# Performance work log

Hardware: AMD Instinct MI355X
Metric: run time of the kernel (lower is better)

Reference implementation:

```python
import jax, jax.numpy as jnp
import numpy as np

HEADS = 20  # SDXL-style: hidden_size 1280 / head_dim 64
IP_SCALE = 1.0


def setup_inputs() -> dict:
    key = jax.random.key(0)
    ks = jax.random.split(key, 12)
    B, Sq, T, C, D, NIP = 4, 4096, 77, 1280, 2048, 16
    s = lambda fan: 1.0 / np.sqrt(fan)
    # post-softmax multiplicative mask: col 0 (sot token) forced to 1, rest a binary spatial mask
    spat = (jax.random.uniform(ks[0], (1, Sq, 1)) < 0.5).astype(jnp.float32)
    attention_mask = jnp.concatenate([jnp.ones((1, Sq, 1)), jnp.tile(spat, (1, 1, T - 1))], axis=-1)
    return {
        "hidden_states": jax.random.normal(ks[1], (B, Sq, C), jnp.float32),
        "encoder_hidden_states": jax.random.normal(ks[2], (B, T, D), jnp.float32),
        "ip_hidden_states": jax.random.normal(ks[3], (B, NIP, D), jnp.float32),
        "attention_mask": attention_mask,
        "Wq": jax.random.normal(ks[4], (C, C), jnp.float32) * s(C),
        "Wk": jax.random.normal(ks[5], (D, C), jnp.float32) * s(D),
        "Wv": jax.random.normal(ks[6], (D, C), jnp.float32) * s(D),
        "Wo": jax.random.normal(ks[7], (C, C), jnp.float32) * s(C),
        "bo": jnp.zeros((C,), jnp.float32),
        "Wk_ip": jax.random.normal(ks[8], (D, C), jnp.float32) * s(D),
        "Wv_ip": jax.random.normal(ks[9], (D, C), jnp.float32) * s(D),
    }


def reference(hidden_states, encoder_hidden_states, ip_hidden_states, attention_mask,
              Wq, Wk, Wv, Wo, bo, Wk_ip, Wv_ip):
    B, Sq, C = hidden_states.shape
    H = HEADS
    d = C // H
    scale = d ** -0.5
    # projections (torch Linear with weights stored [in, out])
    q = (hidden_states @ Wq).reshape(B, Sq, H, d)
    k = (encoder_hidden_states @ Wk).reshape(B, -1, H, d)
    v = (encoder_hidden_states @ Wv).reshape(B, -1, H, d)
    # explicit QK^T softmax, then POST-softmax multiplicative mask (as in get_attention_scores + mask multiply)
    scores = jnp.einsum('bqhd,bkhd->bhqk', q, k) * scale
    probs = jax.nn.softmax(scores, axis=-1)
    probs = probs * attention_mask[:, None, :, :]  # [1,1,Sq,T] broadcast over batch*heads
    out = jnp.einsum('bhqk,bkhd->bqhd', probs, v).reshape(B, Sq, C)
    out = out @ Wo + bo  # to_out[0]; to_out[1] is dropout (identity at eval)
    # IP-adapter stream (single stream, no spatial ip mask): standard SDPA against ip tokens
    k_ip = (ip_hidden_states @ Wk_ip).reshape(B, -1, H, d)
    v_ip = (ip_hidden_states @ Wv_ip).reshape(B, -1, H, d)
    s_ip = jnp.einsum('bqhd,bkhd->bhqk', q, k_ip) * scale
    p_ip = jax.nn.softmax(s_ip, axis=-1)
    ip_out = jnp.einsum('bhqk,bkhd->bqhd', p_ip, v_ip).reshape(B, Sq, C)
    return out + IP_SCALE * ip_out
```

## Files before the change

kernel.cpp:

```cpp
#include <hip/hip_runtime.h>

typedef __attribute__((ext_vector_type(4))) float f32x4;
typedef __attribute__((ext_vector_type(8))) short s16x8;
typedef __attribute__((ext_vector_type(8))) __bf16 bf16x8;
typedef unsigned short u16;

__device__ __forceinline__ u16 f2b(float f) {
  union { float f; unsigned u; } x; x.f = f;
  unsigned r = x.u + 0x7fffu + ((x.u >> 16) & 1u);
  return (u16)(r >> 16);
}
__device__ __forceinline__ float b2f(u16 u) {
  union { unsigned u; float f; } x; x.u = ((unsigned)u) << 16;
  return x.f;
}
__device__ __forceinline__ void gld16(const void* g, void* l) {
  __builtin_amdgcn_global_load_lds(
      (const __attribute__((address_space(1))) unsigned int*)g,
      (__attribute__((address_space(3))) unsigned int*)l, 16, 0, 0);
}
__device__ __forceinline__ f32x4 mfma_bf16(s16x8 a, s16x8 b, f32x4 c) {
  return __builtin_amdgcn_mfma_f32_16x16x32_bf16(
      __builtin_bit_cast(bf16x8, a), __builtin_bit_cast(bf16x8, b), c, 0, 0, 0);
}

#define BAR() asm volatile("s_barrier" ::: "memory")

__global__ void k_convert_all(const float* __restrict__ hs, const float* __restrict__ ehs,
                              const float* __restrict__ iph,
                              u16* __restrict__ hsb, u16* __restrict__ ehsb,
                              u16* __restrict__ ipb) {
  const int n1 = 16384 * 1280 / 4, n2 = 308 * 2048 / 4, n3 = 64 * 2048 / 4;
  int i = blockIdx.x * blockDim.x + threadIdx.x;
  const float* src; u16* dst; int j = i;
  if (i < n1) { src = hs; dst = hsb; }
  else if (i < n1 + n2) { src = ehs; dst = ehsb; j = i - n1; }
  else if (i < n1 + n2 + n3) { src = iph; dst = ipb; j = i - n1 - n2; }
  else return;
  float4 v = ((const float4*)src)[j];
  ushort4 o;
  o.x = f2b(v.x); o.y = f2b(v.y); o.z = f2b(v.z); o.w = f2b(v.w);
  ((ushort4*)dst)[j] = o;
}

__global__ void k_transpose_all(const float* Wk, const float* Wv, const float* Wkip,
                                const float* Wvip, const float* Wq, const float* Wo,
                                u16* TK, u16* TV, u16* TKip, u16* TVip,
                                u16* TQ, u16* TO) {
  const int z = blockIdx.z;
  const float* W = (z == 0) ? Wk : (z == 1) ? Wv : (z == 2) ? Wkip
                  : (z == 3) ? Wvip : (z == 4) ? Wq : Wo;
  u16* T = (z == 0) ? TK : (z == 1) ? TV : (z == 2) ? TKip
          : (z == 3) ? TVip : (z == 4) ? TQ : TO;
  const int K = (z < 4) ? 2048 : 1280;
  const int N = 1280;
  __shared__ float tile[32][33];
  int n0 = blockIdx.x * 32, k0 = blockIdx.y * 32;
  if (k0 >= K) return;
  int tx = threadIdx.x & 31, ty = threadIdx.x >> 5;
#pragma unroll
  for (int i = 0; i < 32; i += 8)
    tile[ty + i][tx] = W[(size_t)(k0 + ty + i) * N + n0 + tx];
  __syncthreads();
#pragma unroll
  for (int i = 0; i < 32; i += 8)
    T[(size_t)(n0 + ty + i) * K + k0 + tx] = f2b(tile[tx][ty + i]);
}

__device__ __forceinline__ void gemm_core0(
    const u16* __restrict__ A, const u16* __restrict__ BT,
    int M, int N, int K, u16* __restrict__ outb, int m0, int n0) {
  const int tid = threadIdx.x;
  const int l = tid & 63;
  const int w = tid >> 6;
  const int wr = w >> 1, wc = w & 1;
  __shared__ u16 As[5][4096];
  __shared__ u16 Bs[5][4096];
  f32x4 acc[4][4] = {};

  const int o0 = tid * 16;
  const int o1 = o0 + 4096;
  const int ra0 = o0 >> 6, ca0 = (o0 & 63) >> 1;
  const int ra1 = o1 >> 6, ca1 = (o1 & 63) >> 1;
  int ga0 = m0 + ra0; if (ga0 >= M) ga0 = M - 1;
  int ga1 = m0 + ra1; if (ga1 >= M) ga1 = M - 1;
  const u16* Ar0 = A + (size_t)ga0 * K + ca0;
  const u16* Ar1 = A + (size_t)ga1 * K + ca1;
  const u16* Br0 = BT + (size_t)(n0 + ra0) * K + ca0;
  const u16* Br1 = BT + (size_t)(n0 + ra1) * K + ca1;

  const int KT = K >> 5;
#define SSTAGE(s, kt)                                 \
  {                                                   \
    const int k0_ = (kt) << 5;                        \
    gld16(Ar0 + k0_, &As[s][o0 >> 1]);                \
    gld16(Ar1 + k0_, &As[s][o1 >> 1]);                \
    gld16(Br0 + k0_, &Bs[s][o0 >> 1]);                \
    gld16(Br1 + k0_, &Bs[s][o1 >> 1]);                \
  }
  SSTAGE(0, 0);
  SSTAGE(1, 1);
  SSTAGE(2, 2);
  SSTAGE(3, 3);
  asm volatile("s_waitcnt vmcnt(12)" ::: "memory");
  BAR();

  int slot = 0, s4 = 4;
  for (int j = 0; j < KT; ++j) {
    if (j + 4 < KT) SSTAGE(s4, j + 4);
    s16x8 af[4], bfr[4];
#pragma unroll
    for (int mi = 0; mi < 4; ++mi)
      af[mi] = *(const s16x8*)&As[slot][(wr * 64 + mi * 16 + (l & 15)) * 32 + (l >> 4) * 8];
#pragma unroll
    for (int ni = 0; ni < 4; ++ni)
      bfr[ni] = *(const s16x8*)&Bs[slot][(wc * 64 + ni * 16 + (l & 15)) * 32 + (l >> 4) * 8];
#pragma unroll
    for (int mi = 0; mi < 4; ++mi)
#pragma unroll
      for (int ni = 0; ni < 4; ++ni)
        acc[mi][ni] = mfma_bf16(af[mi], bfr[ni], acc[mi][ni]);
    const int rem = KT - 2 - j;
    if (rem >= 3)      asm volatile("s_waitcnt vmcnt(12)" ::: "memory");
    else if (rem == 2) asm volatile("s_waitcnt vmcnt(8)" ::: "memory");
    else if (rem == 1) asm volatile("s_waitcnt vmcnt(4)" ::: "memory");
    else               asm volatile("s_waitcnt vmcnt(0)" ::: "memory");
    BAR();
    ++slot; if (slot >= 5) slot = 0;
    ++s4; if (s4 >= 5) s4 = 0;
  }

#pragma unroll
  for (int mi = 0; mi < 4; ++mi) {
    const int mbase = m0 + wr * 64 + mi * 16 + (l >> 4) * 4;
#pragma unroll
    for (int ni = 0; ni < 4; ++ni) {
      const int ncol = n0 + wc * 64 + ni * 16 + (l & 15);
#pragma unroll
      for (int r = 0; r < 4; ++r) {
        int m = mbase + r;
        if (m < M) outb[(size_t)m * N + ncol] = f2b(acc[mi][ni][r]);
      }
    }
  }
#undef SSTAGE
}

__global__ __launch_bounds__(256) void k_gemm_small4(
    const u16* __restrict__ ehsb, const u16* __restrict__ ipb,
    const u16* __restrict__ WkT, const u16* __restrict__ WvT,
    const u16* __restrict__ WkipT, const u16* __restrict__ WvipT,
    u16* kbuf, u16* vbuf, u16* kipb, u16* vipb) {
  const int z = blockIdx.z;
  const int M = (z < 2) ? 308 : 64;
  const int m0 = blockIdx.y * 128;
  if (m0 >= M) return;
  const u16* A = (z < 2) ? ehsb : ipb;
  const u16* BT = (z == 0) ? WkT : (z == 1) ? WvT : (z == 2) ? WkipT : WvipT;
  u16* out = (z == 0) ? kbuf : (z == 1) ? vbuf : (z == 2) ? kipb : vipb;
  gemm_core0(A, BT, M, 1280, 2048, out, m0, blockIdx.x * 128);
}

__global__ void k_vtrans(const u16* __restrict__ vbuf, const u16* __restrict__ vipb,
                         u16* __restrict__ vt, u16* __restrict__ vipt) {
  const int b = blockIdx.x, h = blockIdx.y, z = blockIdx.z;
  const int tid = threadIdx.x;
  __shared__ u16 tile[80][72];
  if (z == 0) {
    for (int s = tid; s < 80 * 8; s += 256) {
      int t = s >> 3, c = s & 7;
      int4 v = {0, 0, 0, 0};
      if (t < 77) v = *(const int4*)(vbuf + (size_t)(b * 77 + t) * 1280 + h * 64 + c * 8);
      *(int4*)&tile[t][c * 8] = v;
    }
    __syncthreads();
    for (int s = tid; s < 64 * 12; s += 256) {
      int d = s / 12, tc = s % 12;
      s16x8 v;
#pragma unroll
      for (int j = 0; j < 8; ++j) {
        int t = tc * 8 + j;
        v[j] = (t < 80) ? (short)tile[t][d] : (short)0;
      }
      *(s16x8*)(vt + ((size_t)(h * 64 + d) * 4 + b) * 96 + tc * 8) = v;
    }
  } else {
    for (int s = tid; s < 16 * 8; s += 256) {
      int t = s >> 3, c = s & 7;
      *(int4*)&tile[t][c * 8] =
          *(const int4*)(vipb + (size_t)(b * 16 + t) * 1280 + h * 64 + c * 8);
    }
    __syncthreads();
    for (int s = tid; s < 64 * 2; s += 256) {
      int d = s >> 1, tc = s & 1;
      s16x8 v;
#pragma unroll
      for (int j = 0; j < 8; ++j) v[j] = (short)tile[tc * 8 + j][d];
      *(s16x8*)(vipt + ((size_t)(h * 64 + d) * 4 + b) * 16 + tc * 8) = v;
    }
  }
}

template <int EPI>
__global__ __launch_bounds__(512, 1) void k_gemm256(
    const u16* __restrict__ A, const u16* __restrict__ BT,
    int N, int K, float alpha,
    u16* __restrict__ outb, float* __restrict__ outf,
    const float* __restrict__ bias, const u16* __restrict__ ipadd,
    int nbx) {
  __shared__ u16 lds[73728];
  const int tid = threadIdx.x, l = tid & 63, w = tid >> 6;
  const int lr = l & 15, lg = l >> 4;
  const int wr = w >> 2, wc = w & 3;
  const bool wlo = (w < 4);

  const int nwg = gridDim.x;
  const int q = nwg >> 3, r = nwg & 7;
  const int xcd = blockIdx.x & 7, lid = blockIdx.x >> 3;
  const int wg = (xcd < r) ? (xcd * (q + 1) + lid)
                           : (r * (q + 1) + (xcd - r) * q + lid);
  const int bm0 = (wg / nbx) * 256, bn0 = (wg % nbx) * 320;

  const int srow = tid >> 2;
  const int sslot = ((tid & 3) ^ ((srow >> 1) & 3)) * 8;
  const size_t aO0 = (size_t)(bm0 + srow) * K + sslot;
  const size_t aO1 = aO0 + (size_t)128 * K;
  const size_t bO0 = (size_t)(bn0 + srow) * K + sslot;
  const size_t bO1 = bO0 + (size_t)128 * K;
  const size_t bO2 = bO0 + (size_t)256 * K;
  const int d0 = tid * 8, d1 = (tid + 512) * 8, d2 = (tid + 1024) * 8;

  const int KT = K >> 5;
  f32x4 acc[8][5] = {};
  s16x8 bfv[5], afv[4];

  const int xsw = (lg ^ ((lr >> 1) & 3)) * 8;
  const int aRow = (wr * 128 + lr) * 32 + xsw;
  const int bRow = 32768 + (wc * 80 + lr) * 32 + xsw;

#define STAGE_A(slot, kt)                                              \
  {                                                                    \
    const int base_ = (slot) * 8192;                                   \
    const size_t go_ = (size_t)(kt) * 32;                              \
    gld16(A + aO0 + go_, &lds[base_ + d0]);                            \
    gld16(A + aO1 + go_, &lds[base_ + d1]);                            \
  }
#define STAGE_B(slot, kt)                                              \
  {                                                                    \
    const int base_ = 32768 + (slot) * 10240;                          \
    const size_t go_ = (size_t)(kt) * 32;                              \
    gld16(BT + bO0 + go_, &lds[base_ + d0]);                           \
    gld16(BT + bO1 + go_, &lds[base_ + d1]);                           \
    if (wlo) gld16(BT + bO2 + go_, &lds[base_ + d2]);                  \
  }
#define WAIT_DEEP()                                                    \
  {                                                                    \
    if (wlo) asm volatile("s_waitcnt vmcnt(10)" ::: "memory");         \
    else     asm volatile("s_waitcnt vmcnt(8)" ::: "memory");          \
  }
#define WAIT_MID()                                                     \
  {                                                                    \
    if (wlo) asm volatile("s_waitcnt vmcnt(5)" ::: "memory");          \
    else     asm volatile("s_waitcnt vmcnt(4)" ::: "memory");          \
  }
#define WAITVM0() asm volatile("s_waitcnt vmcnt(0)" ::: "memory")

  STAGE_A(0, 0); STAGE_B(0, 0);
  STAGE_A(1, 1); STAGE_B(1, 1);
  STAGE_A(2, 2); STAGE_B(2, 2);
  WAIT_DEEP();
  BAR();

  for (int j = 0; j < KT; ++j) {
    const int slot = j & 3;
    const int ab = slot * 8192;
    const int bb = slot * 10240;
    const bool pf = (j + 3 < KT);
    const int s3 = (j + 3) & 3;
#pragma unroll
    for (int ni = 0; ni < 5; ++ni)
      bfv[ni] = *(const s16x8*)&lds[bb + bRow + ni * 512];
#pragma unroll
    for (int mi = 0; mi < 4; ++mi)
      afv[mi] = *(const s16x8*)&lds[ab + aRow + mi * 512];
    if (pf) STAGE_A(s3, j + 3);
    __builtin_amdgcn_s_setprio(1);
#pragma unroll
    for (int mi = 0; mi < 4; ++mi)
#pragma unroll
      for (int ni = 0; ni < 5; ++ni)
        acc[mi][ni] = mfma_bf16(afv[mi], bfv[ni], acc[mi][ni]);
    __builtin_amdgcn_s_setprio(0);
#pragma unroll
    for (int mi = 0; mi < 4; ++mi)
      afv[mi] = *(const s16x8*)&lds[ab + aRow + (mi + 4) * 512];
    if (pf) STAGE_B(s3, j + 3);
    __builtin_amdgcn_s_setprio(1);
#pragma unroll
    for (int mi = 0; mi < 4; ++mi)
#pragma unroll
      for (int ni = 0; ni < 5; ++ni)
        acc[mi + 4][ni] = mfma_bf16(afv[mi], bfv[ni], acc[mi + 4][ni]);
    __builtin_amdgcn_s_setprio(0);
    if (pf) { WAIT_DEEP(); }
    else if (j == KT - 3) { WAIT_MID(); }
    else { WAITVM0(); }
    BAR();
  }

  WAITVM0();
  __syncthreads();

  if constexpr (EPI == 0) {
#pragma unroll
    for (int half = 0; half < 2; ++half) {
      if (half) __syncthreads();
      if (wr == half) {
#pragma unroll
        for (int mi = 0; mi < 8; ++mi) {
          const int row = mi * 16 + lg * 4;
#pragma unroll
          for (int ni = 0; ni < 5; ++ni) {
            const int col = wc * 80 + ni * 16 + lr;
#pragma unroll
            for (int rr = 0; rr < 4; ++rr)
              lds[(row + rr) * 320 + col] = f2b(acc[mi][ni][rr] * alpha);
          }
        }
      }
      __syncthreads();
      const int rbase = tid >> 3;
      const int cseg = tid & 7;
#pragma unroll
      for (int rr2 = 0; rr2 < 2; ++rr2)
#pragma unroll
        for (int jj = 0; jj < 5; ++jj) {
          const int row = rr2 * 64 + rbase;
          const int ch = cseg + jj * 8;
          *(int4*)(outb + (size_t)(bm0 + half * 128 + row) * N + bn0 + ch * 8) =
              *(const int4*)&lds[row * 320 + ch * 8];
        }
    }
  } else {
#pragma unroll
    for (int mi = 0; mi < 8; ++mi) {
      const int mrow = bm0 + wr * 128 + mi * 16 + lg * 4;
#pragma unroll
      for (int ni = 0; ni < 5; ++ni) {
        const int ncol = bn0 + wc * 80 + ni * 16 + lr;
#pragma unroll
        for (int rr = 0; rr < 4; ++rr) {
          const size_t idx = (size_t)(mrow + rr) * N + ncol;
          outf[idx] = acc[mi][ni][rr] + bias[ncol] + b2f(ipadd[idx]);
        }
      }
    }
  }
#undef STAGE_A
#undef STAGE_B
#undef WAIT_DEEP
#undef WAIT_MID
#undef WAITVM0
}

__global__ __launch_bounds__(512, 4) void k_attn(
    const u16* __restrict__ Q,
    const u16* __restrict__ Kb,
    const u16* __restrict__ Kip,
    const u16* __restrict__ Vt,
    const u16* __restrict__ VipT,
    const float* __restrict__ mask,
    u16* __restrict__ Oattn, u16* __restrict__ Oip) {
  const int qt = blockIdx.x, h = blockIdx.y, b = blockIdx.z;
  const int tid = threadIdx.x, l = tid & 63, w = tid >> 6;
  const int lr = l & 15, lg = l >> 4;
  const int r0 = w * 16;
  const int m0 = b * 4096 + qt * 128;

  __shared__ u16 S[34560];
  u16 (*Ks)[72] = (u16(*)[72]) & S[0];
  const int VT_OFF = 6912, VIP_OFF = 13568;
  u16 (*Ps)[104] = (u16(*)[104]) & S[16128];
  u16 (*P2s)[40] = (u16(*)[40]) & S[29440];

  const u16* qrow = Q + (size_t)(m0 + r0 + lr) * 1280 + h * 64;
  s16x8 aq0 = *(const s16x8*)(qrow + lg * 8);
  s16x8 aq1 = *(const s16x8*)(qrow + 32 + lg * 8);

  for (int s = tid; s < 96 * 8; s += 512) {
    const int row = s >> 3, seg = s & 7;
    int4 v = {0, 0, 0, 0};
    if (row < 77)
      v = *(const int4*)(Kb + (size_t)(b * 77 + row) * 1280 + h * 64 + seg * 8);
    else if (row >= 80)
      v = *(const int4*)(Kip + (size_t)(b * 16 + row - 80) * 1280 + h * 64 + seg * 8);
    *(int4*)&Ks[row][(seg ^ ((row >> 3) & 3)) * 8] = v;
  }
  for (int s = tid; s < 64 * 12; s += 512) {
    const int row = s / 12, c = s % 12;
    *(int4*)&S[VT_OFF + row * 104 + c * 8] =
        *(const int4*)(Vt + ((size_t)(h * 64 + row) * 4 + b) * 96 + c * 8);
  }
  for (int s = tid; s < 64 * 4; s += 512) {
    const int row = s >> 2, c = s & 3;
    int4 v = {0, 0, 0, 0};
    if (c >= 2)
      v = *(const int4*)(VipT + ((size_t)(h * 64 + row) * 4 + b) * 16 + (c - 2) * 8);
    *(int4*)&S[VIP_OFF + row * 40 + c * 8] = v;
  }
  __syncthreads();

  f32x4 sc[5];
  f32x4 sip = {};
#pragma unroll
  for (int t5 = 0; t5 < 6; ++t5) {
    const int trow = t5 * 16 + lr;
    const int qz = (trow >> 3) & 3;
    s16x8 b0 = *(const s16x8*)&Ks[trow][(lg ^ qz) * 8];
    s16x8 b1 = *(const s16x8*)&Ks[trow][((lg + 4) ^ qz) * 8];
    f32x4 c = {};
    c = mfma_bf16(aq0, b0, c);
    c = mfma_bf16(aq1, b1, c);
    if (t5 < 5) sc[t5] = c; else sip = c;
  }

#pragma unroll
  for (int r = 0; r < 4; ++r) {
    float mx = fmaxf(fmaxf(fmaxf(sc[0][r], sc[1][r]), fmaxf(sc[2][r], sc[3][r])), sc[4][r]);
    mx = fmaxf(mx, __shfl_xor(mx, 1));
    mx = fmaxf(mx, __shfl_xor(mx, 2));
    mx = fmaxf(mx, __shfl_xor(mx, 4));
    mx = fmaxf(mx, __shfl_xor(mx, 8));
    float p[5], sm = 0.f;
#pragma unroll
    for (int t5 = 0; t5 < 5; ++t5) {
      bool valid = (t5 < 4) | (lr < 13);
      p[t5] = valid ? __expf(sc[t5][r] - mx) : 0.f;
      sm += p[t5];
    }
    sm += __shfl_xor(sm, 1);
    sm += __shfl_xor(sm, 2);
    sm += __shfl_xor(sm, 4);
    sm += __shfl_xor(sm, 8);
    const float inv = 1.0f / sm;
    const int row = r0 + lg * 4 + r;
    const int qg = qt * 128 + row;
#pragma unroll
    for (int t5 = 0; t5 < 5; ++t5) {
      int t = t5 * 16 + lr;
      float pf = 0.f;
      if (t < 77) pf = p[t5] * inv * mask[qg * 77 + t];
      Ps[row][t] = f2b(pf);
    }
    Ps[row][80 + lr] = 0;

    float m2 = sip[r];
    m2 = fmaxf(m2, __shfl_xor(m2, 1));
    m2 = fmaxf(m2, __shfl_xor(m2, 2));
    m2 = fmaxf(m2, __shfl_xor(m2, 4));
    m2 = fmaxf(m2, __shfl_xor(m2, 8));
    float pi = __expf(sip[r] - m2);
    float s2 = pi;
    s2 += __shfl_xor(s2, 1);
    s2 += __shfl_xor(s2, 2);
    s2 += __shfl_xor(s2, 4);
    s2 += __shfl_xor(s2, 8);
    P2s[row][lr] = 0;
    P2s[row][16 + lr] = f2b(pi / s2);
  }

  s16x8 ap[3];
#pragma unroll
  for (int ks = 0; ks < 3; ++ks)
    ap[ks] = *(const s16x8*)&Ps[r0 + lr][ks * 32 + lg * 8];
  s16x8 aip = *(const s16x8*)&P2s[r0 + lr][lg * 8];

  f32x4 om[4], oi[4];
#pragma unroll
  for (int nt = 0; nt < 4; ++nt) {
    const int vrow = nt * 16 + lr;
    f32x4 o = {};
#pragma unroll
    for (int ks = 0; ks < 3; ++ks) {
      s16x8 bv = *(const s16x8*)&S[VT_OFF + vrow * 104 + (ks * 4 + lg) * 8];
      o = mfma_bf16(ap[ks], bv, o);
    }
    s16x8 bip = *(const s16x8*)&S[VIP_OFF + vrow * 40 + lg * 8];
    f32x4 o2 = {};
    o2 = mfma_bf16(aip, bip, o2);
    om[nt] = o;
    oi[nt] = o2;
  }

  __syncthreads();

  u16 (*Om)[72] = (u16(*)[72]) & S[0];
  u16 (*Oi)[72] = (u16(*)[72]) & S[16128];
#pragma unroll
  for (int nt = 0; nt < 4; ++nt)
#pragma unroll
    for (int r = 0; r < 4; ++r) {
      const int row = r0 + lg * 4 + r;
      const int d = nt * 16 + lr;
      Om[row][d] = f2b(om[nt][r]);
      Oi[row][d] = f2b(oi[nt][r]);
    }
  __syncthreads();

  for (int s = tid; s < 128 * 8; s += 512) {
    const int row = s >> 3, seg = s & 7;
    const size_t g = (size_t)(m0 + row) * 1280 + h * 64 + seg * 8;
    *(int4*)(Oattn + g) = *(const int4*)&Om[row][seg * 8];
    *(int4*)(Oip + g) = *(const int4*)&Oi[row][seg * 8];
  }
}

extern "C" void kernel_launch(void* const* d_in, const int* in_sizes, int n_in,
                              void* d_out, int out_size, void* d_ws, size_t ws_size,
                              hipStream_t stream) {
  (void)in_sizes; (void)n_in; (void)out_size; (void)ws_size;
  const float* hs   = (const float*)d_in[0];
  const float* ehs  = (const float*)d_in[1];
  const float* iph  = (const float*)d_in[2];
  const float* mask = (const float*)d_in[3];
  const float* Wq   = (const float*)d_in[4];
  const float* Wk   = (const float*)d_in[5];
  const float* Wv   = (const float*)d_in[6];
  const float* Wo   = (const float*)d_in[7];
  const float* bo   = (const float*)d_in[8];
  const float* Wkip = (const float*)d_in[9];
  const float* Wvip = (const float*)d_in[10];
  float* out = (float*)d_out;

  char* ws = (char*)d_ws;
  size_t off = 0;
  auto alloc = [&](size_t bytes) {
    char* p = ws + off;
    off += (bytes + 255) & ~(size_t)255;
    return p;
  };
  u16* hsb   = (u16*)alloc(16384ull * 1280 * 2);
  u16* qbuf  = (u16*)alloc(16384ull * 1280 * 2);
  u16* ipout = (u16*)alloc(16384ull * 1280 * 2);
  u16* WqT   = (u16*)alloc(1280ull * 1280 * 2);
  u16* WoT   = (u16*)alloc(1280ull * 1280 * 2);
  u16* WkT   = (u16*)alloc(1280ull * 2048 * 2);
  u16* WvT   = (u16*)alloc(1280ull * 2048 * 2);
  u16* WkipT = (u16*)alloc(1280ull * 2048 * 2);
  u16* WvipT = (u16*)alloc(1280ull * 2048 * 2);
  u16* ehsb  = (u16*)alloc(308ull * 2048 * 2);
  u16* ipb   = (u16*)alloc(64ull * 2048 * 2);
  u16* kbuf  = (u16*)alloc(308ull * 1280 * 2);
  u16* vbuf  = (u16*)alloc(308ull * 1280 * 2);
  u16* kipb  = (u16*)alloc(64ull * 1280 * 2);
  u16* vipb  = (u16*)alloc(64ull * 1280 * 2);
  u16* vt    = (u16*)alloc(1280ull * 4 * 96 * 2);
  u16* vipt  = (u16*)alloc(1280ull * 4 * 16 * 2);

  const int ntot4 = (16384 * 1280 + 308 * 2048 + 64 * 2048) / 4;
  k_convert_all<<<(ntot4 + 255) / 256, 256, 0, stream>>>(hs, ehs, iph, hsb, ehsb, ipb);
  k_transpose_all<<<dim3(40, 64, 6), 256, 0, stream>>>(Wk, Wv, Wkip, Wvip, Wq, Wo,
                                                       WkT, WvT, WkipT, WvipT, WqT, WoT);

  k_gemm256<0><<<256, 512, 0, stream>>>(hsb, WqT, 1280, 1280, 0.125f,
                                        qbuf, nullptr, nullptr, nullptr, 4);
  k_gemm_small4<<<dim3(10, 3, 4), 256, 0, stream>>>(ehsb, ipb, WkT, WvT, WkipT, WvipT,
                                                    kbuf, vbuf, kipb, vipb);
  k_vtrans<<<dim3(4, 20, 2), 256, 0, stream>>>(vbuf, vipb, vt, vipt);

  k_attn<<<dim3(32, 20, 4), 512, 0, stream>>>(qbuf, kbuf, kipb, vt, vipt, mask,
                                              hsb, ipout);

  k_gemm256<1><<<256, 512, 0, stream>>>(hsb, WoT, 1280, 1280, 1.f,
                                        nullptr, out, bo, ipout, 4);
}
```

Measured before the change: 267.5 us.

## Restructure GEMM main loop into double-buffered 64-wide K steps with barrier phases

Replaces the 4-slot, 3-deep prefetch ring over 32-wide K tiles with two ping-pong buffers, each holding a 64-wide K step made of two 32-wide sub-tiles. Each iteration now runs four MFMA phases separated by extra barriers and explicit lgkmcnt waits, in the style of a ping-pong schedule. The aim is to interleave the global-to-LDS loads with compute more tightly. The cost is more barriers per K step and a prefetch depth of only one step, which may expose memory latency.

```diff
diff --git a/kernel.cpp b/kernel.cpp
--- a/kernel.cpp
+++ b/kernel.cpp
@@ -230,85 +230,117 @@
   const size_t bO2 = bO0 + (size_t)256 * K;
   const int d0 = tid * 8, d1 = (tid + 512) * 8, d2 = (tid + 1024) * 8;
 
-  const int KT = K >> 5;
+  const int KT = K >> 6;
   f32x4 acc[8][5] = {};
   s16x8 bfv[5], afv[4];
 
   const int xsw = (lg ^ ((lr >> 1) & 3)) * 8;
-  const int aRow = (wr * 128 + lr) * 32 + xsw;
-  const int bRow = 32768 + (wc * 80 + lr) * 32 + xsw;
-
-#define STAGE_A(slot, kt)                                              \
+  const int aRowOff = (wr * 128 + lr) * 32 + xsw;
+  const int bRowOff = (wc * 80 + lr) * 32 + xsw;
+
+#define STAGE_AQ(bufb, kk, kt)                                         \
   {                                                                    \
-    const int base_ = (slot) * 8192;                                   \
-    const size_t go_ = (size_t)(kt) * 32;                              \
+    const int base_ = (bufb) + (kk) * 8192;                            \
+    const size_t go_ = (size_t)(kt) * 64 + (kk) * 32;                  \
     gld16(A + aO0 + go_, &lds[base_ + d0]);                            \
     gld16(A + aO1 + go_, &lds[base_ + d1]);                            \
   }
-#define STAGE_B(slot, kt)                                              \
+#define STAGE_BQ(bufb, kk, kt)                                         \
   {                                                                    \
-    const int base_ = 32768 + (slot) * 10240;                          \
-    const size_t go_ = (size_t)(kt) * 32;                              \
+    const int base_ = (bufb) + 16384 + (kk) * 10240;                   \
+    const size_t go_ = (size_t)(kt) * 64 + (kk) * 32;                  \
     gld16(BT + bO0 + go_, &lds[base_ + d0]);                           \
     gld16(BT + bO1 + go_, &lds[base_ + d1]);                           \
     if (wlo) gld16(BT + bO2 + go_, &lds[base_ + d2]);                  \
   }
-#define WAIT_DEEP()                                                    \
-  {                                                                    \
-    if (wlo) asm volatile("s_waitcnt vmcnt(10)" ::: "memory");         \
-    else     asm volatile("s_waitcnt vmcnt(8)" ::: "memory");          \
-  }
-#define WAIT_MID()                                                     \
+#define WAITQ()                                                        \
   {                                                                    \
     if (wlo) asm volatile("s_waitcnt vmcnt(5)" ::: "memory");          \
     else     asm volatile("s_waitcnt vmcnt(4)" ::: "memory");          \
   }
-#define WAITVM0() asm volatile("s_waitcnt vmcnt(0)" ::: "memory")
-
-  STAGE_A(0, 0); STAGE_B(0, 0);
-  STAGE_A(1, 1); STAGE_B(1, 1);
-  STAGE_A(2, 2); STAGE_B(2, 2);
-  WAIT_DEEP();
+#define VM0() asm volatile("s_waitcnt vmcnt(0)" ::: "memory")
+#define LGKM0() asm volatile("s_waitcnt lgkmcnt(0)" ::: "memory")
+#define PRIO1() __builtin_amdgcn_s_setprio(1)
+#define PRIO0() __builtin_amdgcn_s_setprio(0)
+
+  STAGE_AQ(0, 0, 0);
+  STAGE_BQ(0, 0, 0);
+  STAGE_AQ(0, 1, 0);
+  STAGE_BQ(0, 1, 0);
+  WAITQ();
   BAR();
 
   for (int j = 0; j < KT; ++j) {
-    const int slot = j & 3;
-    const int ab = slot * 8192;
-    const int bb = slot * 10240;
-    const bool pf = (j + 3 < KT);
-    const int s3 = (j + 3) & 3;
+    const int cb = (j & 1) * 36864;
+    const int nb = 36864 - cb;
+    const bool pf = (j + 1 < KT);
 #pragma unroll
     for (int ni = 0; ni < 5; ++ni)
-      bfv[ni] = *(const s16x8*)&lds[bb + bRow + ni * 512];
-#pragma unroll
-    for (int mi = 0; mi < 4; ++mi)
-      afv[mi] = *(const s16x8*)&lds[ab + aRow + mi * 512];
-    if (pf) STAGE_A(s3, j + 3);
-    __builtin_amdgcn_s_setprio(1);
+      bfv[ni] = *(const s16x8*)&lds[cb + 16384 + bRowOff + ni * 512];
+#pragma unroll
+    for (int mi = 0; mi < 4; ++mi)
+      afv[mi] = *(const s16x8*)&lds[cb + aRowOff + mi * 512];
+    if (pf) STAGE_AQ(nb, 0, j + 1);
+    BAR();
+    LGKM0();
+    PRIO1();
 #pragma unroll
     for (int mi = 0; mi < 4; ++mi)
 #pragma unroll
       for (int ni = 0; ni < 5; ++ni)
         acc[mi][ni] = mfma_bf16(afv[mi], bfv[ni], acc[mi][ni]);
-    __builtin_amdgcn_s_setprio(0);
-#pragma unroll
-    for (int mi = 0; mi < 4; ++mi)
-      afv[mi] = *(const s16x8*)&lds[ab + aRow + (mi + 4) * 512];
-    if (pf) STAGE_B(s3, j + 3);
-    __builtin_amdgcn_s_setprio(1);
+    PRIO0();
+    BAR();
+#pragma unroll
+    for (int mi = 0; mi < 4; ++mi)
+      afv[mi] = *(const s16x8*)&lds[cb + aRowOff + (mi + 4) * 512];
+    if (pf) STAGE_BQ(nb, 0, j + 1);
+    BAR();
+    LGKM0();
+    PRIO1();
 #pragma unroll
     for (int mi = 0; mi < 4; ++mi)
 #pragma unroll
       for (int ni = 0; ni < 5; ++ni)
         acc[mi + 4][ni] = mfma_bf16(afv[mi], bfv[ni], acc[mi + 4][ni]);
-    __builtin_amdgcn_s_setprio(0);
-    if (pf) { WAIT_DEEP(); }
-    else if (j == KT - 3) { WAIT_MID(); }
-    else { WAITVM0(); }
-    BAR();
-  }
-
-  WAITVM0();
+    PRIO0();
+    if (pf) { WAITQ(); } else { VM0(); }
+    BAR();
+#pragma unroll
+    for (int ni = 0; ni < 5; ++ni)
+      bfv[ni] = *(const s16x8*)&lds[cb + 16384 + 10240 + bRowOff + ni * 512];
+#pragma unroll
+    for (int mi = 0; mi < 4; ++mi)
+      afv[mi] = *(const s16x8*)&lds[cb + 8192 + aRowOff + mi * 512];
+    if (pf) STAGE_AQ(nb, 1, j + 1);
+    BAR();
+    LGKM0();
+    PRIO1();
+#pragma unroll
+    for (int mi = 0; mi < 4; ++mi)
+#pragma unroll
+      for (int ni = 0; ni < 5; ++ni)
+        acc[mi][ni] = mfma_bf16(afv[mi], bfv[ni], acc[mi][ni]);
+    PRIO0();
+    BAR();
+#pragma unroll
+    for (int mi = 0; mi < 4; ++mi)
+      afv[mi] = *(const s16x8*)&lds[cb + 8192 + aRowOff + (mi + 4) * 512];
+    if (pf) STAGE_BQ(nb, 1, j + 1);
+    BAR();
+    LGKM0();
+    PRIO1();
+#pragma unroll
+    for (int mi = 0; mi < 4; ++mi)
+#pragma unroll
+      for (int ni = 0; ni < 5; ++ni)
+        acc[mi + 4][ni] = mfma_bf16(afv[mi], bfv[ni], acc[mi + 4][ni]);
+    PRIO0();
+    if (pf) { WAITQ(); } else { VM0(); }
+    BAR();
+  }
+
+  VM0();
   __syncthreads();
 
   if constexpr (EPI == 0) {
@@ -356,11 +388,13 @@
       }
     }
   }
-#undef STAGE_A
-#undef STAGE_B
-#undef WAIT_DEEP
-#undef WAIT_MID
-#undef WAITVM0
+#undef STAGE_AQ
+#undef STAGE_BQ
+#undef WAITQ
+#undef VM0
+#undef LGKM0
+#undef PRIO1
+#undef PRIO0
 }
 
 __global__ __launch_bounds__(512, 4) void k_attn(
```

Result: no change. 269.8 us (+0.9%).
